# Optimization experiments

Hardware: AMD Instinct MI355X
Metric: run time of the kernel (lower is better)

Reference implementation:

```python
import jax, jax.numpy as jnp
import numpy as np

DECAY_MIN = 0.9
DECAY_MAX = 0.999

def setup_inputs() -> dict:
    key = jax.random.key(0)
    ks = jax.random.split(key, 6)
    B, L, D, M = 8, 4096, 1024, 64
    s = 0.02
    return {
        "x": jax.random.normal(ks[0], (B, L, D), jnp.float32),
        "Wq": jax.random.normal(ks[1], (D, M), jnp.float32) * s,
        "Wk": jax.random.normal(ks[2], (D, M), jnp.float32) * s,
        "Wv": jax.random.normal(ks[3], (D, M), jnp.float32) * s,
        "Wo": jax.random.normal(ks[4], (M, D), jnp.float32) * s,
        "bo": jnp.zeros((D,), jnp.float32),
        "Wg": jax.random.normal(ks[5], (D, 1), jnp.float32) * s,
        "bg": jnp.zeros((1,), jnp.float32),
        "decay_param": jnp.full((1,), 0.5, jnp.float32),
    }

def reference(x, Wq, Wk, Wv, Wo, bo, Wg, bg, decay_param):
    B, L, D = x.shape
    M = Wq.shape[1]
    # decay in [DECAY_MIN, DECAY_MAX], shape (1,) -> scalar broadcast
    decay = DECAY_MIN + jax.nn.sigmoid(decay_param) * (DECAY_MAX - DECAY_MIN)
    q = x @ Wq  # (B,L,M)
    k = x @ Wk
    v = x @ Wv
    gates = jax.nn.sigmoid(x @ Wg + bg)[..., 0]  # (B,L)
    S0 = jnp.zeros((B, M, M), x.dtype)

    def scan_fn(S, inp):
        q_t, k_t, v_t, g_t = inp  # (B,M),(B,M),(B,M),(B,)
        gk = k_t * g_t[:, None]
        gv = v_t * g_t[:, None]
        # fast-weight update: S = decay*S + gk ⊗ gv
        S = decay * S + gk[:, :, None] * gv[:, None, :]
        out_t = jnp.einsum('bd,bde->be', q_t, S)
        return S, out_t

    S_final, outs = jax.lax.scan(
        scan_fn, S0,
        (q.transpose(1, 0, 2), k.transpose(1, 0, 2), v.transpose(1, 0, 2), gates.T))
    outs = outs.transpose(1, 0, 2)  # (B,L,M)
    y = outs @ Wo + bo  # (B,L,D); dropout deterministic (eval)
    return y, S_final
```

## Files before the change

kernel.cpp:

```cpp
#include <hip/hip_runtime.h>
#include <math.h>

#define B_SZ 8
#define L_SZ 4096
#define D_SZ 1024
#define M_SZ 64
#define ROWS (B_SZ * L_SZ)
#define NCHUNK 64
#define CHUNK 64

#define FMA4(acc, sc, v) { (acc).x += (sc)*(v).x; (acc).y += (sc)*(v).y; (acc).z += (sc)*(v).z; (acc).w += (sc)*(v).w; }
#define SCALE4(v, sc) { (v).x *= (sc); (v).y *= (sc); (v).z *= (sc); (v).w *= (sc); }

typedef __attribute__((ext_vector_type(8))) short bf16x8;
typedef __attribute__((ext_vector_type(4))) float f32x4;

__device__ __forceinline__ float sigmoid_f(float z) { return 1.0f / (1.0f + __expf(-z)); }
__device__ __forceinline__ float decay_of(const float* __restrict__ dp) {
  return 0.9f + (0.999f - 0.9f) * sigmoid_f(dp[0]);
}
__device__ __forceinline__ unsigned short f2bf(float f) {
  unsigned int u = __float_as_uint(f);
  unsigned int r = (u + 0x7FFFu + ((u >> 16) & 1u)) >> 16;
  return (unsigned short)r;
}

__global__ __launch_bounds__(256) void k0_prep(
    const float* __restrict__ Wq, const float* __restrict__ Wk,
    const float* __restrict__ Wv, unsigned short* __restrict__ Wt)
{
  const int n = blockIdx.x;
  const float* src = (n < 64) ? Wq : (n < 128) ? Wk : Wv;
  const int nc = n & 63;
  #pragma unroll
  for (int j = 0; j < 4; ++j) {
    int k = threadIdx.x + 256 * j;
    Wt[(size_t)n * D_SZ + k] = f2bf(src[(size_t)k * 64 + nc]);
  }
}

#define K1_ROWS 64
#define K1_LDB 72

__global__ __launch_bounds__(256, 2) void k1_qkvg_mfma(
    const float* __restrict__ x, const unsigned short* __restrict__ Wt,
    const float* __restrict__ Wg, const float* __restrict__ bg,
    float* __restrict__ q_ws, float* __restrict__ a_ws, float* __restrict__ b_ws)
{
  __shared__ __align__(16) unsigned short Bs[2][192 * K1_LDB];
  __shared__ float Wgs[D_SZ];

  const int tid  = threadIdx.x;
  const int lane = tid & 63;
  const int w    = tid >> 6;
  const int quad = lane >> 4;
  const int l15  = lane & 15;
  const int row0 = blockIdx.x * K1_ROWS;

  const float* xrow = x + (size_t)(row0 + 16 * w + l15) * D_SZ;

  f32x4 acc[12];
  #pragma unroll
  for (int tn = 0; tn < 12; ++tn) acc[tn] = (f32x4){0.f, 0.f, 0.f, 0.f};

  uint4  bb[6];
  float4 xa[4];
  bf16x8 af[2];
  float  gacc = 0.f;

  *reinterpret_cast<float4*>(&Wgs[4 * tid]) = *reinterpret_cast<const float4*>(Wg + 4 * tid);

  auto loadB = [&](int k0) {
    #pragma unroll
    for (int i = 0; i < 6; ++i) {
      int cid = tid + 256 * i;
      int n = cid >> 3, c = cid & 7;
      bb[i] = *reinterpret_cast<const uint4*>(Wt + (size_t)n * D_SZ + k0 + 8 * c);
    }
  };
  auto loadA = [&](int k0) {
    #pragma unroll
    for (int kt = 0; kt < 2; ++kt)
      #pragma unroll
      for (int j = 0; j < 2; ++j)
        xa[kt * 2 + j] = *reinterpret_cast<const float4*>(xrow + k0 + kt * 32 + quad * 8 + 4 * j);
  };
  auto writeB = [&](int buf) {
    #pragma unroll
    for (int i = 0; i < 6; ++i) {
      int cid = tid + 256 * i;
      int n = cid >> 3, c = cid & 7;
      *reinterpret_cast<uint4*>(&Bs[buf][n * K1_LDB + 8 * c]) = bb[i];
    }
  };
  auto cvtA = [&](int k0) {
    #pragma unroll
    for (int kt = 0; kt < 2; ++kt) {
      float4 lo = xa[kt * 2], hi = xa[kt * 2 + 1];
      const float* wp = &Wgs[k0 + kt * 32 + quad * 8];
      float4 w0 = *reinterpret_cast<const float4*>(wp);
      float4 w1 = *reinterpret_cast<const float4*>(wp + 4);
      gacc += lo.x * w0.x + lo.y * w0.y + lo.z * w0.z + lo.w * w0.w
            + hi.x * w1.x + hi.y * w1.y + hi.z * w1.z + hi.w * w1.w;
      uint4 p;
      p.x = (unsigned)f2bf(lo.x) | ((unsigned)f2bf(lo.y) << 16);
      p.y = (unsigned)f2bf(lo.z) | ((unsigned)f2bf(lo.w) << 16);
      p.z = (unsigned)f2bf(hi.x) | ((unsigned)f2bf(hi.y) << 16);
      p.w = (unsigned)f2bf(hi.z) | ((unsigned)f2bf(hi.w) << 16);
      af[kt] = *reinterpret_cast<bf16x8*>(&p);
    }
  };

  loadA(0); loadB(0);
  __syncthreads();
  writeB(0);
  cvtA(0);
  __syncthreads();

  for (int t = 0; t < 16; ++t) {
    const int cur = t & 1;
    if (t < 15) { loadA((t + 1) * 64); loadB((t + 1) * 64); }
    #pragma unroll
    for (int tn = 0; tn < 12; ++tn) {
      bf16x8 b0 = *reinterpret_cast<bf16x8*>(&Bs[cur][(tn * 16 + l15) * K1_LDB + quad * 8]);
      bf16x8 b1 = *reinterpret_cast<bf16x8*>(&Bs[cur][(tn * 16 + l15) * K1_LDB + 32 + quad * 8]);
      acc[tn] = __builtin_amdgcn_mfma_f32_16x16x32_bf16(af[0], b0, acc[tn], 0, 0, 0);
      acc[tn] = __builtin_amdgcn_mfma_f32_16x16x32_bf16(af[1], b1, acc[tn], 0, 0, 0);
    }
    if (t < 15) {
      writeB(cur ^ 1);
      cvtA((t + 1) * 64);
      __syncthreads();
    }
  }

  float g = gacc;
  g += __shfl_xor(g, 16);
  g += __shfl_xor(g, 32);
  const float gs = sigmoid_f(g + bg[0]);
  float gr[4];
  #pragma unroll
  for (int r = 0; r < 4; ++r) gr[r] = __shfl(gs, quad * 4 + r);

  #pragma unroll
  for (int tn = 0; tn < 12; ++tn) {
    const int ncol = (tn & 3) * 16 + l15;
    float* dst = (tn < 4) ? q_ws : (tn < 8 ? a_ws : b_ws);
    #pragma unroll
    for (int r = 0; r < 4; ++r) {
      const int rl = 16 * w + quad * 4 + r;
      float vv = acc[tn][r];
      if (tn >= 4) vv *= gr[r];
      dst[(size_t)(row0 + rl) * 64 + ncol] = vv;
    }
  }
}

__global__ __launch_bounds__(256) void k2_delta(
    const float* __restrict__ a_ws, const float* __restrict__ b_ws,
    const float* __restrict__ dp, float* __restrict__ dS)
{
  __shared__ float Aa[64][64];
  __shared__ float Bc[64][64];
  __shared__ float pw[64];
  const int tid = threadIdx.x;
  const int bc = blockIdx.x;
  const int rowbase = (bc >> 6) * L_SZ + (bc & 63) * CHUNK;
  const int s = tid >> 2, m0 = (tid & 3) * 16;
  #pragma unroll
  for (int j = 0; j < 4; ++j) {
    *reinterpret_cast<float4*>(&Aa[s][m0 + 4*j]) =
        *reinterpret_cast<const float4*>(&a_ws[(size_t)(rowbase + s) * 64 + m0 + 4*j]);
    *reinterpret_cast<float4*>(&Bc[s][m0 + 4*j]) =
        *reinterpret_cast<const float4*>(&b_ws[(size_t)(rowbase + s) * 64 + m0 + 4*j]);
  }
  if (tid < 64) pw[tid] = powf(decay_of(dp), (float)(63 - tid));
  __syncthreads();
  const int d0 = tid >> 2, e0 = (tid & 3) * 16;
  float4 o0 = make_float4(0,0,0,0), o1 = o0, o2 = o0, o3 = o0;
  for (int ss = 0; ss < 64; ++ss) {
    float wa = pw[ss] * Aa[ss][d0];
    float4 b0 = *reinterpret_cast<float4*>(&Bc[ss][e0+0]);
    float4 b1 = *reinterpret_cast<float4*>(&Bc[ss][e0+4]);
    float4 b2 = *reinterpret_cast<float4*>(&Bc[ss][e0+8]);
    float4 b3 = *reinterpret_cast<float4*>(&Bc[ss][e0+12]);
    FMA4(o0, wa, b0); FMA4(o1, wa, b1); FMA4(o2, wa, b2); FMA4(o3, wa, b3);
  }
  float* dst = &dS[((size_t)bc << 12) + d0 * 64 + e0];
  *reinterpret_cast<float4*>(dst + 0)  = o0;
  *reinterpret_cast<float4*>(dst + 4)  = o1;
  *reinterpret_cast<float4*>(dst + 8)  = o2;
  *reinterpret_cast<float4*>(dst + 12) = o3;
}

__global__ __launch_bounds__(256) void k3_scan(
    const float* __restrict__ dS, const float* __restrict__ dp,
    float* __restrict__ Sst, float* __restrict__ sfin)
{
  const int g = blockIdx.x * 256 + threadIdx.x;
  const int b = g >> 12;
  const int de = g & 4095;
  const float dC = powf(decay_of(dp), 64.0f);
  const size_t base = ((size_t)(b * 64) << 12) + de;
  float d[NCHUNK];
  #pragma unroll
  for (int c = 0; c < NCHUNK; ++c) d[c] = dS[base + ((size_t)c << 12)];
  float s = 0.f;
  #pragma unroll
  for (int c = 0; c < NCHUNK; ++c) {
    Sst[base + ((size_t)c << 12)] = s;
    s = dC * s + d[c];
  }
  sfin[((size_t)b << 12) + de] = s;
}

__global__ __launch_bounds__(256) void k4_intra(
    const float* __restrict__ q_ws, const float* __restrict__ a_ws,
    const float* __restrict__ b_ws, const float* __restrict__ Sst,
    const float* __restrict__ dp, float* __restrict__ outs)
{
  __shared__ float Qs[64][68];
  __shared__ float Ps[64][68];
  __shared__ float Bs[64][64];
  __shared__ float S0s[64][64];
  __shared__ float pw[65];
  const int tid = threadIdx.x;
  const int bc = blockIdx.x;
  const int rowbase = (bc >> 6) * L_SZ + (bc & 63) * CHUNK;
  const int s = tid >> 2, m0 = (tid & 3) * 16;
  #pragma unroll
  for (int j = 0; j < 4; ++j) {
    float4 qv = *reinterpret_cast<const float4*>(&q_ws[(size_t)(rowbase + s) * 64 + m0 + 4*j]);
    Qs[s][m0+4*j+0] = qv.x; Qs[s][m0+4*j+1] = qv.y; Qs[s][m0+4*j+2] = qv.z; Qs[s][m0+4*j+3] = qv.w;
    float4 av = *reinterpret_cast<const float4*>(&a_ws[(size_t)(rowbase + s) * 64 + m0 + 4*j]);
    Ps[m0+4*j+0][s] = av.x; Ps[m0+4*j+1][s] = av.y; Ps[m0+4*j+2][s] = av.z; Ps[m0+4*j+3][s] = av.w;
    float4 bv = *reinterpret_cast<const float4*>(&b_ws[(size_t)(rowbase + s) * 64 + m0 + 4*j]);
    *reinterpret_cast<float4*>(&Bs[s][m0+4*j]) = bv;
    float4 sv = *reinterpret_cast<const float4*>(&Sst[((size_t)bc << 12) + tid*16 + 4*j]);
    *reinterpret_cast<float4*>(&(&S0s[0][0])[tid*16 + 4*j]) = sv;
  }
  if (tid < 65) pw[tid] = powf(decay_of(dp), (float)tid);
  __syncthreads();

  const int t0 = tid >> 2, c0 = (tid & 3) * 16;
  float4 r0 = make_float4(0,0,0,0), r1 = r0, r2 = r0, r3 = r0;
  for (int m = 0; m < 64; ++m) {
    float qv = Qs[t0][m];
    float4 a0 = *reinterpret_cast<float4*>(&Ps[m][c0+0]);
    float4 a1 = *reinterpret_cast<float4*>(&Ps[m][c0+4]);
    float4 a2 = *reinterpret_cast<float4*>(&Ps[m][c0+8]);
    float4 a3 = *reinterpret_cast<float4*>(&Ps[m][c0+12]);
    FMA4(r0, qv, a0); FMA4(r1, qv, a1); FMA4(r2, qv, a2); FMA4(r3, qv, a3);
  }
  float rr[16] = {r0.x,r0.y,r0.z,r0.w, r1.x,r1.y,r1.z,r1.w,
                  r2.x,r2.y,r2.z,r2.w, r3.x,r3.y,r3.z,r3.w};
  __syncthreads();
  #pragma unroll
  for (int j = 0; j < 16; ++j) {
    const int sidx = c0 + j;
    Ps[t0][sidx] = (sidx <= t0) ? rr[j] * pw[t0 - sidx] : 0.f;
  }
  __syncthreads();

  float4 o0 = make_float4(0,0,0,0), o1 = o0, o2 = o0, o3 = o0;
  for (int m = 0; m < 64; ++m) {
    float qv = Qs[t0][m];
    float4 v0 = *reinterpret_cast<float4*>(&S0s[m][c0+0]);
    float4 v1 = *reinterpret_cast<float4*>(&S0s[m][c0+4]);
    float4 v2 = *reinterpret_cast<float4*>(&S0s[m][c0+8]);
    float4 v3 = *reinterpret_cast<float4*>(&S0s[m][c0+12]);
    FMA4(o0, qv, v0); FMA4(o1, qv, v1); FMA4(o2, qv, v2); FMA4(o3, qv, v3);
  }
  const float dsc = pw[t0 + 1];
  SCALE4(o0, dsc); SCALE4(o1, dsc); SCALE4(o2, dsc); SCALE4(o3, dsc);
  for (int ss = 0; ss < 64; ++ss) {
    float pv = Ps[t0][ss];
    float4 b0 = *reinterpret_cast<float4*>(&Bs[ss][c0+0]);
    float4 b1 = *reinterpret_cast<float4*>(&Bs[ss][c0+4]);
    float4 b2 = *reinterpret_cast<float4*>(&Bs[ss][c0+8]);
    float4 b3 = *reinterpret_cast<float4*>(&Bs[ss][c0+12]);
    FMA4(o0, pv, b0); FMA4(o1, pv, b1); FMA4(o2, pv, b2); FMA4(o3, pv, b3);
  }
  float* dst = &outs[(size_t)(rowbase + t0) * 64 + c0];
  *reinterpret_cast<float4*>(dst + 0)  = o0;
  *reinterpret_cast<float4*>(dst + 4)  = o1;
  *reinterpret_cast<float4*>(dst + 8)  = o2;
  *reinterpret_cast<float4*>(dst + 12) = o3;
}

__global__ __launch_bounds__(256) void k5_proj(
    const float* __restrict__ outs, const float* __restrict__ Wo,
    const float* __restrict__ bo, float* __restrict__ y)
{
  __shared__ float Os[64][68];
  __shared__ float Ws[64][64];
  const int tid = threadIdx.x;
  const int tx = tid & 15, ty = tid >> 4;
  const int row0 = blockIdx.x * 64;
  const int n0 = blockIdx.y * 64;
  const int s = tid >> 2, m0 = (tid & 3) * 16;
  #pragma unroll
  for (int j = 0; j < 4; ++j) {
    float4 ov = *reinterpret_cast<const float4*>(&outs[(size_t)(row0 + s) * 64 + m0 + 4*j]);
    Os[s][m0+4*j+0] = ov.x; Os[s][m0+4*j+1] = ov.y; Os[s][m0+4*j+2] = ov.z; Os[s][m0+4*j+3] = ov.w;
    float4 wv = *reinterpret_cast<const float4*>(&Wo[(size_t)s * D_SZ + n0 + m0 + 4*j]);
    *reinterpret_cast<float4*>(&Ws[s][m0+4*j]) = wv;
  }
  __syncthreads();
  float4 acc[4];
  #pragma unroll
  for (int r = 0; r < 4; ++r) acc[r] = make_float4(0,0,0,0);
  for (int kk = 0; kk < 64; ++kk) {
    float a0 = Os[4*ty+0][kk];
    float a1 = Os[4*ty+1][kk];
    float a2 = Os[4*ty+2][kk];
    float a3 = Os[4*ty+3][kk];
    float4 w = *reinterpret_cast<float4*>(&Ws[kk][4*tx]);
    FMA4(acc[0], a0, w); FMA4(acc[1], a1, w); FMA4(acc[2], a2, w); FMA4(acc[3], a3, w);
  }
  float4 bv = *reinterpret_cast<const float4*>(&bo[n0 + 4*tx]);
  #pragma unroll
  for (int r = 0; r < 4; ++r) {
    float4 res;
    res.x = acc[r].x + bv.x; res.y = acc[r].y + bv.y;
    res.z = acc[r].z + bv.z; res.w = acc[r].w + bv.w;
    *reinterpret_cast<float4*>(&y[(size_t)(row0 + 4*ty + r) * D_SZ + n0 + 4*tx]) = res;
  }
}

extern "C" void kernel_launch(void* const* d_in, const int* in_sizes, int n_in,
                              void* d_out, int out_size, void* d_ws, size_t ws_size,
                              hipStream_t stream) {
  (void)in_sizes; (void)n_in; (void)out_size; (void)ws_size;
  const float* x  = (const float*)d_in[0];
  const float* Wq = (const float*)d_in[1];
  const float* Wk = (const float*)d_in[2];
  const float* Wv = (const float*)d_in[3];
  const float* Wo = (const float*)d_in[4];
  const float* bo = (const float*)d_in[5];
  const float* Wg = (const float*)d_in[6];
  const float* bg = (const float*)d_in[7];
  const float* dp = (const float*)d_in[8];

  float* y    = (float*)d_out;
  float* sfin = y + (size_t)B_SZ * L_SZ * D_SZ;

  float* ws   = (float*)d_ws;
  const size_t SEG = (size_t)ROWS * M_SZ;
  float* q_ws = ws;
  float* a_ws = q_ws + SEG;
  float* b_ws = a_ws + SEG;
  float* dS   = b_ws + SEG;
  float* Sst  = dS   + SEG;
  float* outs = Sst  + SEG;
  unsigned short* Wt = (unsigned short*)outs;

  k0_prep<<<dim3(192), dim3(256), 0, stream>>>(Wq, Wk, Wv, Wt);
  k1_qkvg_mfma<<<dim3(ROWS / K1_ROWS), dim3(256), 0, stream>>>(x, Wt, Wg, bg, q_ws, a_ws, b_ws);
  k2_delta<<<dim3(B_SZ * NCHUNK), dim3(256), 0, stream>>>(a_ws, b_ws, dp, dS);
  k3_scan<<<dim3((B_SZ * M_SZ * M_SZ) / 256), dim3(256), 0, stream>>>(dS, dp, Sst, sfin);
  k4_intra<<<dim3(B_SZ * NCHUNK), dim3(256), 0, stream>>>(q_ws, a_ws, b_ws, Sst, dp, outs);
  k5_proj<<<dim3(ROWS / 64, D_SZ / 64), dim3(256), 0, stream>>>(outs, Wo, bo, y);
}
```

Before: 374.6 us.

## Stream QKV projection tiles via direct global-to-LDS loads and fold gate into MFMA

The QKV+gate projection kernel now loads x and the weights straight into LDS with global_load_lds, replacing the register-staged double buffer. The prep kernel pre-tiles the weights into a padded per-k-tile layout and appends Wg as an extra 13th MFMA column tile, which removes the scalar gate dot product. Outputs are staged through LDS so the stores are coalesced float4 writes, and occupancy is raised to 3 blocks. The cost is losing the explicit load/compute overlap: the loop now waits on a barrier each tile. The change also pads the k5 LDS tile differently.

```diff
diff --git a/kernel.cpp b/kernel.cpp
--- a/kernel.cpp
+++ b/kernel.cpp
@@ -25,30 +25,52 @@
   return (unsigned short)r;
 }
 
+__device__ __forceinline__ void gl2lds16(const void* g, void* l) {
+  __builtin_amdgcn_global_load_lds(
+      (const __attribute__((address_space(1))) unsigned int*)g,
+      (__attribute__((address_space(3))) unsigned int*)l, 16, 0, 0);
+}
+
+#define BT_CH     1872
+#define BT_CH_PAD 1920
+#define BT_BYTES  (BT_CH_PAD * 16)
 __global__ __launch_bounds__(256) void k0_prep(
     const float* __restrict__ Wq, const float* __restrict__ Wk,
-    const float* __restrict__ Wv, unsigned short* __restrict__ Wt)
+    const float* __restrict__ Wv, const float* __restrict__ Wg,
+    unsigned short* __restrict__ Wt)
 {
   const int n = blockIdx.x;
-  const float* src = (n < 64) ? Wq : (n < 128) ? Wk : Wv;
-  const int nc = n & 63;
-  #pragma unroll
-  for (int j = 0; j < 4; ++j) {
-    int k = threadIdx.x + 256 * j;
-    Wt[(size_t)n * D_SZ + k] = f2bf(src[(size_t)k * 64 + nc]);
+  #pragma unroll
+  for (int j = 0; j < 5; ++j) {
+    int idx = threadIdx.x + 256 * j;
+    if (idx < 1152) {
+      int kt = idx / 72;
+      int r  = idx - kt * 72;
+      int c = r >> 3, e = r & 7;
+      float v = 0.f;
+      if (c < 8 && n < 193) {
+        int k = kt * 64 + c * 8 + e;
+        v = (n < 64)  ? Wq[(size_t)k * 64 + n]
+          : (n < 128) ? Wk[(size_t)k * 64 + (n - 64)]
+          : (n < 192) ? Wv[(size_t)k * 64 + (n - 128)]
+                      : Wg[k];
+      }
+      Wt[((size_t)kt * BT_CH_PAD + (size_t)n * 9 + c) * 8 + e] = f2bf(v);
+    }
   }
 }
 
 #define K1_ROWS 64
-#define K1_LDB 72
-
-__global__ __launch_bounds__(256, 2) void k1_qkvg_mfma(
+#define A_STRIDE 272
+#define B_STRIDE 144
+
+__global__ __launch_bounds__(256, 3) void k1_qkvg_mfma(
     const float* __restrict__ x, const unsigned short* __restrict__ Wt,
-    const float* __restrict__ Wg, const float* __restrict__ bg,
+    const float* __restrict__ bg,
     float* __restrict__ q_ws, float* __restrict__ a_ws, float* __restrict__ b_ws)
 {
-  __shared__ __align__(16) unsigned short Bs[2][192 * K1_LDB];
-  __shared__ float Wgs[D_SZ];
+  __shared__ __align__(16) unsigned char AsB[K1_ROWS * A_STRIDE];
+  __shared__ __align__(16) unsigned char BsB[BT_BYTES];
 
   const int tid  = threadIdx.x;
   const int lane = tid & 63;
@@ -57,51 +79,43 @@
   const int l15  = lane & 15;
   const int row0 = blockIdx.x * K1_ROWS;
 
-  const float* xrow = x + (size_t)(row0 + 16 * w + l15) * D_SZ;
-
-  f32x4 acc[12];
-  #pragma unroll
-  for (int tn = 0; tn < 12; ++tn) acc[tn] = (f32x4){0.f, 0.f, 0.f, 0.f};
-
-  uint4  bb[6];
-  float4 xa[4];
-  bf16x8 af[2];
-  float  gacc = 0.f;
-
-  *reinterpret_cast<float4*>(&Wgs[4 * tid]) = *reinterpret_cast<const float4*>(Wg + 4 * tid);
-
-  auto loadB = [&](int k0) {
-    #pragma unroll
-    for (int i = 0; i < 6; ++i) {
-      int cid = tid + 256 * i;
-      int n = cid >> 3, c = cid & 7;
-      bb[i] = *reinterpret_cast<const uint4*>(Wt + (size_t)n * D_SZ + k0 + 8 * c);
-    }
-  };
-  auto loadA = [&](int k0) {
-    #pragma unroll
-    for (int kt = 0; kt < 2; ++kt)
-      #pragma unroll
-      for (int j = 0; j < 2; ++j)
-        xa[kt * 2 + j] = *reinterpret_cast<const float4*>(xrow + k0 + kt * 32 + quad * 8 + 4 * j);
-  };
-  auto writeB = [&](int buf) {
-    #pragma unroll
-    for (int i = 0; i < 6; ++i) {
-      int cid = tid + 256 * i;
-      int n = cid >> 3, c = cid & 7;
-      *reinterpret_cast<uint4*>(&Bs[buf][n * K1_LDB + 8 * c]) = bb[i];
-    }
-  };
-  auto cvtA = [&](int k0) {
+  const unsigned char* xb  = (const unsigned char*)(x + (size_t)row0 * D_SZ);
+  const unsigned char* wtb = (const unsigned char*)Wt;
+
+  const unsigned char* xA[5];
+  #pragma unroll
+  for (int i = 0; i < 5; ++i) {
+    int ci  = i * 256 + tid;
+    int row = ci / 17;
+    int c17 = ci - row * 17;
+    xA[i] = xb + (size_t)row * 4096 + (c17 < 16 ? c17 * 16 : 0);
+  }
+
+  f32x4 acc[13];
+  #pragma unroll
+  for (int tn = 0; tn < 13; ++tn) acc[tn] = (f32x4){0.f, 0.f, 0.f, 0.f};
+
+  for (int t = 0; t < 16; ++t) {
+    #pragma unroll
+    for (int i = 0; i < 4; ++i)
+      gl2lds16(xA[i] + (size_t)t * 256, AsB + (i * 256 + tid) * 16);
+    if (tid < 64)
+      gl2lds16(xA[4] + (size_t)t * 256, AsB + (4 * 256 + tid) * 16);
+    const unsigned char* wt_t = wtb + (size_t)t * BT_BYTES;
+    #pragma unroll
+    for (int i = 0; i < 7; ++i)
+      gl2lds16(wt_t + (i * 256 + tid) * 16, BsB + (i * 256 + tid) * 16);
+    if (tid < 128)
+      gl2lds16(wt_t + (7 * 256 + tid) * 16, BsB + (7 * 256 + tid) * 16);
+
+    __syncthreads();
+
+    bf16x8 af[2];
     #pragma unroll
     for (int kt = 0; kt < 2; ++kt) {
-      float4 lo = xa[kt * 2], hi = xa[kt * 2 + 1];
-      const float* wp = &Wgs[k0 + kt * 32 + quad * 8];
-      float4 w0 = *reinterpret_cast<const float4*>(wp);
-      float4 w1 = *reinterpret_cast<const float4*>(wp + 4);
-      gacc += lo.x * w0.x + lo.y * w0.y + lo.z * w0.z + lo.w * w0.w
-            + hi.x * w1.x + hi.y * w1.y + hi.z * w1.z + hi.w * w1.w;
+      const unsigned char* ap = AsB + (16 * w + l15) * A_STRIDE + kt * 128 + quad * 32;
+      float4 lo = *reinterpret_cast<const float4*>(ap);
+      float4 hi = *reinterpret_cast<const float4*>(ap + 16);
       uint4 p;
       p.x = (unsigned)f2bf(lo.x) | ((unsigned)f2bf(lo.y) << 16);
       p.y = (unsigned)f2bf(lo.z) | ((unsigned)f2bf(lo.w) << 16);
@@ -109,50 +123,49 @@
       p.w = (unsigned)f2bf(hi.z) | ((unsigned)f2bf(hi.w) << 16);
       af[kt] = *reinterpret_cast<bf16x8*>(&p);
     }
-  };
-
-  loadA(0); loadB(0);
-  __syncthreads();
-  writeB(0);
-  cvtA(0);
-  __syncthreads();
-
-  for (int t = 0; t < 16; ++t) {
-    const int cur = t & 1;
-    if (t < 15) { loadA((t + 1) * 64); loadB((t + 1) * 64); }
-    #pragma unroll
-    for (int tn = 0; tn < 12; ++tn) {
-      bf16x8 b0 = *reinterpret_cast<bf16x8*>(&Bs[cur][(tn * 16 + l15) * K1_LDB + quad * 8]);
-      bf16x8 b1 = *reinterpret_cast<bf16x8*>(&Bs[cur][(tn * 16 + l15) * K1_LDB + 32 + quad * 8]);
-      acc[tn] = __builtin_amdgcn_mfma_f32_16x16x32_bf16(af[0], b0, acc[tn], 0, 0, 0);
-      acc[tn] = __builtin_amdgcn_mfma_f32_16x16x32_bf16(af[1], b1, acc[tn], 0, 0, 0);
+    #pragma unroll
+    for (int tn = 0; tn < 13; ++tn) {
+      #pragma unroll
+      for (int kt = 0; kt < 2; ++kt) {
+        bf16x8 bf = *reinterpret_cast<const bf16x8*>(
+            BsB + (tn * 16 + l15) * B_STRIDE + kt * 64 + quad * 16);
+        acc[tn] = __builtin_amdgcn_mfma_f32_16x16x32_bf16(af[kt], bf, acc[tn], 0, 0, 0);
+      }
     }
-    if (t < 15) {
-      writeB(cur ^ 1);
-      cvtA((t + 1) * 64);
-      __syncthreads();
+    __syncthreads();
+  }
+
+  const float bg0 = bg[0];
+  float g4[4];
+  #pragma unroll
+  for (int r = 0; r < 4; ++r) {
+    float gv = __shfl(acc[12][r], lane & 48);
+    g4[r] = sigmoid_f(gv + bg0);
+  }
+
+  float (*T)[68] = (float(*)[68])AsB;
+  const int erow = tid >> 2, eq4 = tid & 3;
+  #pragma unroll
+  for (int p = 0; p < 3; ++p) {
+    float* dst = (p == 0) ? q_ws : (p == 1) ? a_ws : b_ws;
+    #pragma unroll
+    for (int tn4 = 0; tn4 < 4; ++tn4) {
+      #pragma unroll
+      for (int r = 0; r < 4; ++r) {
+        float v = acc[p * 4 + tn4][r];
+        if (p > 0) v *= g4[r];
+        T[16 * w + quad * 4 + r][tn4 * 16 + l15] = v;
+      }
     }
-  }
-
-  float g = gacc;
-  g += __shfl_xor(g, 16);
-  g += __shfl_xor(g, 32);
-  const float gs = sigmoid_f(g + bg[0]);
-  float gr[4];
-  #pragma unroll
-  for (int r = 0; r < 4; ++r) gr[r] = __shfl(gs, quad * 4 + r);
-
-  #pragma unroll
-  for (int tn = 0; tn < 12; ++tn) {
-    const int ncol = (tn & 3) * 16 + l15;
-    float* dst = (tn < 4) ? q_ws : (tn < 8 ? a_ws : b_ws);
-    #pragma unroll
-    for (int r = 0; r < 4; ++r) {
-      const int rl = 16 * w + quad * 4 + r;
-      float vv = acc[tn][r];
-      if (tn >= 4) vv *= gr[r];
-      dst[(size_t)(row0 + rl) * 64 + ncol] = vv;
-    }
+    __syncthreads();
+    float4 vv[4];
+    #pragma unroll
+    for (int j = 0; j < 4; ++j)
+      vv[j] = *reinterpret_cast<float4*>(&T[erow][eq4 * 16 + 4 * j]);
+    #pragma unroll
+    for (int j = 0; j < 4; ++j)
+      *reinterpret_cast<float4*>(&dst[(size_t)(row0 + erow) * 64 + eq4 * 16 + 4 * j]) = vv[j];
+    if (p < 2) __syncthreads();
   }
 }
 
@@ -292,7 +305,7 @@
     const float* __restrict__ outs, const float* __restrict__ Wo,
     const float* __restrict__ bo, float* __restrict__ y)
 {
-  __shared__ float Os[64][68];
+  __shared__ float Os[64][65];
   __shared__ float Ws[64][64];
   const int tid = threadIdx.x;
   const int tx = tid & 15, ty = tid >> 4;
@@ -355,8 +368,8 @@
   float* outs = Sst  + SEG;
   unsigned short* Wt = (unsigned short*)outs;
 
-  k0_prep<<<dim3(192), dim3(256), 0, stream>>>(Wq, Wk, Wv, Wt);
-  k1_qkvg_mfma<<<dim3(ROWS / K1_ROWS), dim3(256), 0, stream>>>(x, Wt, Wg, bg, q_ws, a_ws, b_ws);
+  k0_prep<<<dim3(208), dim3(256), 0, stream>>>(Wq, Wk, Wv, Wg, Wt);
+  k1_qkvg_mfma<<<dim3(ROWS / K1_ROWS), dim3(256), 0, stream>>>(x, Wt, bg, q_ws, a_ws, b_ws);
   k2_delta<<<dim3(B_SZ * NCHUNK), dim3(256), 0, stream>>>(a_ws, b_ws, dp, dS);
   k3_scan<<<dim3((B_SZ * M_SZ * M_SZ) / 256), dim3(256), 0, stream>>>(dS, dp, Sst, sfin);
   k4_intra<<<dim3(B_SZ * NCHUNK), dim3(256), 0, stream>>>(q_ws, a_ws, b_ws, Sst, dp, outs);
```

After: 358.5 us. -4.3%, faster.
